# Kernel optimization log

Measured on AMD Instinct MI355X. Metric: run time of the kernel, lower is better.

## Reference

```python
import jax, jax.numpy as jnp
import numpy as np

B, L, N = 512, 512, 128


def setup_inputs() -> dict:
    key = jax.random.key(0)
    k1, k2, k3, k4 = jax.random.split(key, 4)
    emission = jax.random.normal(k1, (B, L, N), dtype=jnp.float32)
    target = jax.random.randint(k2, (B, L), 0, N, dtype=jnp.int32)
    mask = jnp.ones((B, L), dtype=jnp.float32)
    # params: uniform(-0.1, 0.1) as in reset_parameters
    start_trans = jax.random.uniform(k3, (N,), minval=-0.1, maxval=0.1, dtype=jnp.float32)
    trans = jax.random.uniform(k4, (N, N), minval=-0.1, maxval=0.1, dtype=jnp.float32)
    return {"emission": emission, "target": target, "mask": mask,
            "start_trans": start_trans, "trans": trans}


def _normalizer(emission, mask, start_trans, trans):
    # scores: [B, N]
    scores0 = start_trans + emission[:, 0]
    em_t = jnp.swapaxes(emission, 0, 1)[1:]          # [L-1, B, N]
    m_t = jnp.swapaxes(mask, 0, 1)[1:, :, None]      # [L-1, B, 1]

    def step(scores, xs):
        em_i, m_i = xs
        nxt = jax.nn.logsumexp(scores[:, :, None] + trans[None], axis=1) + em_i
        nxt = m_i * nxt + (1.0 - m_i) * scores
        return nxt, None

    final, _ = jax.lax.scan(step, scores0, (em_t, m_t))
    return jax.nn.logsumexp(final, axis=1)            # [B]


def _path_score(emission, target, mask, start_trans, trans):
    # mask*next + (1-mask)*scores == scores + mask*increment -> fully vectorizable
    b = jnp.arange(emission.shape[0])
    t0 = target[:, 0]
    s0 = start_trans[t0] + emission[b, 0, t0]                         # [B]
    prev, cur = target[:, :-1], target[:, 1:]                         # [B, L-1]
    em_gather = jnp.take_along_axis(emission[:, 1:], cur[:, :, None], axis=2)[..., 0]
    inc = trans[prev, cur] + em_gather                                # [B, L-1]
    return s0 + jnp.sum(mask[:, 1:] * inc, axis=1)                    # [B]


def reference(emission, target, mask, start_trans, trans):
    path_scores = _path_score(emission, target, mask, start_trans, trans)
    normalizer = _normalizer(emission, mask, start_trans, trans)
    return jnp.mean(normalizer - path_scores)
```

## Files before the change

kernel.cpp:

```cpp
#include <hip/hip_runtime.h>

#define B_ 512
#define L_ 512
#define N_ 128
#define TM 256
#define C_BIAS 3.0f

typedef _Float16 h2_t __attribute__((ext_vector_type(2)));

__device__ __forceinline__ float dot2f(h2_t a, h2_t b, float c) {
#if __has_builtin(__builtin_amdgcn_fdot2)
    return __builtin_amdgcn_fdot2(a, b, c, false);
#else
    return c + (float)a[0] * (float)b[0] + (float)a[1] * (float)b[1];
#endif
}

#define DPP_STEP_MAX(v, ctrl)                                                   \
    {                                                                           \
        int _t = __builtin_amdgcn_update_dpp(__float_as_int(v),                 \
                    __float_as_int(v), ctrl, 0xf, 0xf, false);                  \
        v = fmaxf(v, __int_as_float(_t));                                       \
    }
#define DPP_STEP_ADD(v, ctrl)                                                   \
    {                                                                           \
        int _t = __builtin_amdgcn_update_dpp(__float_as_int(v),                 \
                    __float_as_int(v), ctrl, 0xf, 0xf, false);                  \
        v = v + __int_as_float(_t);                                             \
    }

__device__ __forceinline__ float wave_max(float v) {
    DPP_STEP_MAX(v, 0xB1);
    DPP_STEP_MAX(v, 0x4E);
    DPP_STEP_MAX(v, 0x141);
    DPP_STEP_MAX(v, 0x140);
    DPP_STEP_MAX(v, 0x142);
    DPP_STEP_MAX(v, 0x143);
    return __int_as_float(__builtin_amdgcn_readlane(__float_as_int(v), 63));
}
__device__ __forceinline__ float wave_sum(float v) {
    DPP_STEP_ADD(v, 0xB1);
    DPP_STEP_ADD(v, 0x4E);
    DPP_STEP_ADD(v, 0x141);
    DPP_STEP_ADD(v, 0x140);
    DPP_STEP_ADD(v, 0x142);
    DPP_STEP_ADD(v, 0x143);
    return __int_as_float(__builtin_amdgcn_readlane(__float_as_int(v), 63));
}

__global__ __launch_bounds__(64) void norm_kernel(
    const float* __restrict__ em, const int* __restrict__ tg,
    const float* __restrict__ mask, const float* __restrict__ st,
    const float* __restrict__ trans,
    float* __restrict__ alpha, float* __restrict__ beta,
    float* __restrict__ pathf, float* __restrict__ pathb)
{
    __shared__ __align__(16) h2_t Eh[64];
    __shared__ float Mlds[TM];

    const int l  = threadIdx.x;
    const int b  = blockIdx.x >> 1;
    const int bw = blockIdx.x & 1;
    const size_t base = (size_t)b * L_ * N_;
    const int bL = b * L_;

    if (bw == 0) {
        float pacc = 0.f;
        for (int t = 1 + l; t < TM; t += 64) {
            int cur  = tg[bL + t];
            int prev = tg[bL + t - 1];
            pacc += mask[bL + t] * (trans[prev * N_ + cur] + em[base + (size_t)t * N_ + cur]);
        }
        pacc = wave_sum(pacc);
        if (l == 0) {
            int t0 = tg[bL];
            pathf[b] = pacc + st[t0] + em[base + t0];
        }

#pragma unroll
        for (int k = 0; k < 4; ++k) Mlds[l + 64 * k] = mask[bL + l + 64 * k];

        h2_t et0[64], et1[64];
#pragma unroll
        for (int k = 0; k < 64; ++k) {
            float2 r0 = *(const float2*)(trans + (2 * k    ) * N_ + 2 * l);
            float2 r1 = *(const float2*)(trans + (2 * k + 1) * N_ + 2 * l);
            h2_t a, c;
            a[0] = (_Float16)__expf(r0.x); a[1] = (_Float16)__expf(r1.x);
            c[0] = (_Float16)__expf(r0.y); c[1] = (_Float16)__expf(r1.y);
            et0[k] = a; et1[k] = c;
        }

        float2 e0 = *(const float2*)(em + base + 2 * l);
        float2 s2 = *(const float2*)(st + 2 * l);
        float ns0 = s2.x + e0.x;
        float ns1 = s2.y + e0.y;
        float Mprev = wave_max(fmaxf(ns0, ns1));
        {
            h2_t eo;
            eo[0] = (_Float16)__expf(ns0 - Mprev - C_BIAS);
            eo[1] = (_Float16)__expf(ns1 - Mprev - C_BIAS);
            Eh[l] = eo;
        }

        float2 pipe0 = *(const float2*)(em + base + (size_t)1 * N_ + 2 * l);
        float2 pipe1 = *(const float2*)(em + base + (size_t)2 * N_ + 2 * l);
        float2 pipe2 = *(const float2*)(em + base + (size_t)3 * N_ + 2 * l);
        float2 pipe3 = *(const float2*)(em + base + (size_t)4 * N_ + 2 * l);

        auto step = [&](int t, float2& slot) {
            float2 emv = slot;
            int tpf = t + 4; if (tpf > TM - 1) tpf = TM - 1;
            slot = *(const float2*)(em + base + (size_t)tpf * N_ + 2 * l);
            float mk = Mlds[t];

            float mx = wave_max(fmaxf(ns0, ns1));

            float a0 = 0.f, a1 = 0.f, a2 = 0.f, a3 = 0.f;
            float c0 = 0.f, c1 = 0.f, c2 = 0.f, c3 = 0.f;
            const float4* E4 = (const float4*)Eh;
#pragma unroll
            for (int r = 0; r < 16; ++r) {
                float4 blk = E4[r];
                const h2_t* e2 = (const h2_t*)&blk;
                a0 = dot2f(e2[0], et0[4 * r + 0], a0);
                a1 = dot2f(e2[1], et0[4 * r + 1], a1);
                a2 = dot2f(e2[2], et0[4 * r + 2], a2);
                a3 = dot2f(e2[3], et0[4 * r + 3], a3);
                c0 = dot2f(e2[0], et1[4 * r + 0], c0);
                c1 = dot2f(e2[1], et1[4 * r + 1], c1);
                c2 = dot2f(e2[2], et1[4 * r + 2], c2);
                c3 = dot2f(e2[3], et1[4 * r + 3], c3);
            }
            float s_0 = (a0 + a1) + (a2 + a3);
            float s_1 = (c0 + c1) + (c2 + c3);

            float badd = Mprev + C_BIAS;
            float nxt0 = __logf(s_0) + badd + emv.x;
            float nxt1 = __logf(s_1) + badd + emv.y;
            float im = 1.f - mk;
            ns0 = mk * nxt0 + im * ns0;
            ns1 = mk * nxt1 + im * ns1;

            Mprev = mx;
            h2_t eo;
            eo[0] = (_Float16)__expf(ns0 - mx - C_BIAS);
            eo[1] = (_Float16)__expf(ns1 - mx - C_BIAS);
            Eh[l] = eo;
        };

        for (int tt = 1; tt + 3 < TM; tt += 4) {
            step(tt    , pipe0);
            step(tt + 1, pipe1);
            step(tt + 2, pipe2);
            step(tt + 3, pipe3);
        }
        step(TM - 3, pipe0);
        step(TM - 2, pipe1);
        step(TM - 1, pipe2);

        *(float2*)(alpha + b * N_ + 2 * l) = make_float2(ns0, ns1);
    } else {
        float pacc = 0.f;
        for (int t = TM + l; t < L_; t += 64) {
            int cur  = tg[bL + t];
            int prev = tg[bL + t - 1];
            pacc += mask[bL + t] * (trans[prev * N_ + cur] + em[base + (size_t)t * N_ + cur]);
        }
        pacc = wave_sum(pacc);
        if (l == 0) pathb[b] = pacc;

#pragma unroll
        for (int k = 0; k < 4; ++k) Mlds[l + 64 * k] = mask[bL + TM + l + 64 * k];

        h2_t er0[64], er1[64];
#pragma unroll
        for (int k4 = 0; k4 < 32; ++k4) {
            float4 q0 = *(const float4*)(trans + (2 * l    ) * N_ + 4 * k4);
            float4 q1 = *(const float4*)(trans + (2 * l + 1) * N_ + 4 * k4);
            h2_t a, c;
            a[0] = (_Float16)__expf(q0.x); a[1] = (_Float16)__expf(q0.y);
            er0[2 * k4] = a;
            a[0] = (_Float16)__expf(q0.z); a[1] = (_Float16)__expf(q0.w);
            er0[2 * k4 + 1] = a;
            c[0] = (_Float16)__expf(q1.x); c[1] = (_Float16)__expf(q1.y);
            er1[2 * k4] = c;
            c[0] = (_Float16)__expf(q1.z); c[1] = (_Float16)__expf(q1.w);
            er1[2 * k4 + 1] = c;
        }

        float2 e0 = *(const float2*)(em + base + (size_t)(L_ - 1) * N_ + 2 * l);
        float b0 = 0.f, b1 = 0.f;
        float v0 = e0.x, v1 = e0.y;
        float Mprev = wave_max(fmaxf(v0, v1));
        {
            h2_t eo;
            eo[0] = (_Float16)__expf(v0 - Mprev - C_BIAS);
            eo[1] = (_Float16)__expf(v1 - Mprev - C_BIAS);
            Eh[l] = eo;
        }

        float2 pipe0 = *(const float2*)(em + base + (size_t)510 * N_ + 2 * l);
        float2 pipe1 = *(const float2*)(em + base + (size_t)509 * N_ + 2 * l);
        float2 pipe2 = *(const float2*)(em + base + (size_t)508 * N_ + 2 * l);
        float2 pipe3 = *(const float2*)(em + base + (size_t)507 * N_ + 2 * l);

        auto step = [&](int t, float2& slot) {
            float2 emt = slot;
            int tpf = t - 4; if (tpf < TM - 1) tpf = TM - 1;
            slot = *(const float2*)(em + base + (size_t)tpf * N_ + 2 * l);
            float mk = Mlds[t + 1 - TM];

            float mx = wave_max(fmaxf(v0, v1));

            float a0 = 0.f, a1 = 0.f, a2 = 0.f, a3 = 0.f;
            float c0 = 0.f, c1 = 0.f, c2 = 0.f, c3 = 0.f;
            const float4* F4 = (const float4*)Eh;
#pragma unroll
            for (int r = 0; r < 16; ++r) {
                float4 blk = F4[r];
                const h2_t* f2 = (const h2_t*)&blk;
                a0 = dot2f(f2[0], er0[4 * r + 0], a0);
                a1 = dot2f(f2[1], er0[4 * r + 1], a1);
                a2 = dot2f(f2[2], er0[4 * r + 2], a2);
                a3 = dot2f(f2[3], er0[4 * r + 3], a3);
                c0 = dot2f(f2[0], er1[4 * r + 0], c0);
                c1 = dot2f(f2[1], er1[4 * r + 1], c1);
                c2 = dot2f(f2[2], er1[4 * r + 2], c2);
                c3 = dot2f(f2[3], er1[4 * r + 3], c3);
            }
            float s_0 = (a0 + a1) + (a2 + a3);
            float s_1 = (c0 + c1) + (c2 + c3);

            float badd = Mprev + C_BIAS;
            float upd0 = __logf(s_0) + badd;
            float upd1 = __logf(s_1) + badd;
            float im = 1.f - mk;
            b0 = mk * upd0 + im * b0;
            b1 = mk * upd1 + im * b1;

            v0 = b0 + emt.x;
            v1 = b1 + emt.y;
            Mprev = mx;
            h2_t eo;
            eo[0] = (_Float16)__expf(v0 - mx - C_BIAS);
            eo[1] = (_Float16)__expf(v1 - mx - C_BIAS);
            Eh[l] = eo;
        };

        for (int tt = 510; tt >= 258; tt -= 4) {
            step(tt    , pipe0);
            step(tt - 1, pipe1);
            step(tt - 2, pipe2);
            step(tt - 3, pipe3);
        }

        *(float2*)(beta + b * N_ + 2 * l) = make_float2(b0, b1);
    }
}

__global__ __launch_bounds__(64) void zres_kernel(
    const float* __restrict__ alpha, const float* __restrict__ beta,
    const float* __restrict__ pathf, const float* __restrict__ pathb,
    float* __restrict__ zres)
{
    const int l = threadIdx.x;
    const int b = blockIdx.x;
    float2 av = *(const float2*)(alpha + b * N_ + 2 * l);
    float2 bv = *(const float2*)(beta  + b * N_ + 2 * l);
    float v0 = av.x + bv.x;
    float v1 = av.y + bv.y;
    float m = wave_max(fmaxf(v0, v1));
    float s = wave_sum(__expf(v0 - m) + __expf(v1 - m));
    if (l == 0) zres[b] = m + __logf(s) - pathf[b] - pathb[b];
}

__global__ __launch_bounds__(64) void mean_kernel(
    const float* __restrict__ zres, float* __restrict__ out)
{
    const int l = threadIdx.x;
    const float4* z4 = (const float4*)zres;
    float4 a = z4[2 * l];
    float4 c = z4[2 * l + 1];
    float acc = ((a.x + a.y) + (a.z + a.w)) + ((c.x + c.y) + (c.z + c.w));
    acc = wave_sum(acc);
    if (l == 0) out[0] = acc * (1.0f / (float)B_);
}

extern "C" void kernel_launch(void* const* d_in, const int* in_sizes, int n_in,
                              void* d_out, int out_size, void* d_ws, size_t ws_size,
                              hipStream_t stream) {
    const float* emission    = (const float*)d_in[0];
    const int*   target      = (const int*)  d_in[1];
    const float* mask        = (const float*)d_in[2];
    const float* start_trans = (const float*)d_in[3];
    const float* trans       = (const float*)d_in[4];
    float* out = (float*)d_out;

    float* ws_f  = (float*)d_ws;
    float* alpha = ws_f;
    float* beta  = ws_f + B_ * N_;
    float* pathf = ws_f + 2 * B_ * N_;
    float* pathb = ws_f + 2 * B_ * N_ + B_;
    float* zres  = ws_f + 2 * B_ * N_ + 2 * B_;

    norm_kernel<<<2 * B_, 64, 0, stream>>>(emission, target, mask, start_trans,
                                           trans, alpha, beta, pathf, pathb);
    zres_kernel<<<B_, 64, 0, stream>>>(alpha, beta, pathf, pathb, zres);
    mean_kernel<<<1, 64, 0, stream>>>(zres, out);
}
```

Baseline: 331.9 us.

## Split each CRF chain over two waves with double-buffered LDS and barriers

```diff
diff --git a/kernel.cpp b/kernel.cpp
--- a/kernel.cpp
+++ b/kernel.cpp
@@ -29,13 +29,17 @@
         v = v + __int_as_float(_t);                                             \
     }
 
-__device__ __forceinline__ float wave_max(float v) {
+__device__ __forceinline__ float wave_max63(float v) {
     DPP_STEP_MAX(v, 0xB1);
     DPP_STEP_MAX(v, 0x4E);
     DPP_STEP_MAX(v, 0x141);
     DPP_STEP_MAX(v, 0x140);
     DPP_STEP_MAX(v, 0x142);
     DPP_STEP_MAX(v, 0x143);
+    return v;
+}
+__device__ __forceinline__ float wave_max(float v) {
+    v = wave_max63(v);
     return __int_as_float(__builtin_amdgcn_readlane(__float_as_int(v), 63));
 }
 __device__ __forceinline__ float wave_sum(float v) {
@@ -48,105 +52,106 @@
     return __int_as_float(__builtin_amdgcn_readlane(__float_as_int(v), 63));
 }
 
-__global__ __launch_bounds__(64) void norm_kernel(
+__device__ __forceinline__ void sync_lds() {
+    asm volatile("s_waitcnt lgkmcnt(0)" ::: "memory");
+    __builtin_amdgcn_s_barrier();
+    asm volatile("" ::: "memory");
+}
+
+__global__ __launch_bounds__(128, 2) void norm_kernel(
     const float* __restrict__ em, const int* __restrict__ tg,
     const float* __restrict__ mask, const float* __restrict__ st,
     const float* __restrict__ trans,
     float* __restrict__ alpha, float* __restrict__ beta,
     float* __restrict__ pathf, float* __restrict__ pathb)
 {
-    __shared__ __align__(16) h2_t Eh[64];
+    __shared__ __align__(16) _Float16 Ebuf[2][128];
     __shared__ float Mlds[TM];
-
-    const int l  = threadIdx.x;
-    const int b  = blockIdx.x >> 1;
-    const int bw = blockIdx.x & 1;
+    __shared__ __align__(8) float Hm[2][2];
+    __shared__ float Psum[2];
+
+    const int tid = threadIdx.x;
+    const int w   = tid >> 6;
+    const int b   = blockIdx.x >> 1;
+    const int bw  = blockIdx.x & 1;
     const size_t base = (size_t)b * L_ * N_;
     const int bL = b * L_;
 
     if (bw == 0) {
         float pacc = 0.f;
-        for (int t = 1 + l; t < TM; t += 64) {
+        for (int t = 1 + tid; t < TM; t += 128) {
             int cur  = tg[bL + t];
             int prev = tg[bL + t - 1];
             pacc += mask[bL + t] * (trans[prev * N_ + cur] + em[base + (size_t)t * N_ + cur]);
         }
         pacc = wave_sum(pacc);
-        if (l == 0) {
+        if ((tid & 63) == 0) Psum[w] = pacc;
+
+#pragma unroll
+        for (int k = 0; k < 2; ++k) Mlds[tid + 128 * k] = mask[bL + tid + 128 * k];
+
+        h2_t et[64];
+#pragma unroll
+        for (int k = 0; k < 64; ++k) {
+            float r0 = trans[(2 * k    ) * N_ + tid];
+            float r1 = trans[(2 * k + 1) * N_ + tid];
+            h2_t a;
+            a[0] = (_Float16)__expf(r0); a[1] = (_Float16)__expf(r1);
+            et[k] = a;
+        }
+
+        float ns = st[tid] + em[base + tid];
+        {
+            float hl = wave_max63(ns);
+            if ((tid & 63) == 63) Hm[0][w] = hl;
+        }
+        sync_lds();
+        float gmax0 = fmaxf(Hm[0][0], Hm[0][1]);
+        float Mprev = gmax0;
+        Ebuf[0][tid] = (_Float16)__expf(ns - gmax0 - C_BIAS);
+        if (tid == 0) {
             int t0 = tg[bL];
-            pathf[b] = pacc + st[t0] + em[base + t0];
-        }
-
-#pragma unroll
-        for (int k = 0; k < 4; ++k) Mlds[l + 64 * k] = mask[bL + l + 64 * k];
-
-        h2_t et0[64], et1[64];
-#pragma unroll
-        for (int k = 0; k < 64; ++k) {
-            float2 r0 = *(const float2*)(trans + (2 * k    ) * N_ + 2 * l);
-            float2 r1 = *(const float2*)(trans + (2 * k + 1) * N_ + 2 * l);
-            h2_t a, c;
-            a[0] = (_Float16)__expf(r0.x); a[1] = (_Float16)__expf(r1.x);
-            c[0] = (_Float16)__expf(r0.y); c[1] = (_Float16)__expf(r1.y);
-            et0[k] = a; et1[k] = c;
-        }
-
-        float2 e0 = *(const float2*)(em + base + 2 * l);
-        float2 s2 = *(const float2*)(st + 2 * l);
-        float ns0 = s2.x + e0.x;
-        float ns1 = s2.y + e0.y;
-        float Mprev = wave_max(fmaxf(ns0, ns1));
-        {
-            h2_t eo;
-            eo[0] = (_Float16)__expf(ns0 - Mprev - C_BIAS);
-            eo[1] = (_Float16)__expf(ns1 - Mprev - C_BIAS);
-            Eh[l] = eo;
-        }
-
-        float2 pipe0 = *(const float2*)(em + base + (size_t)1 * N_ + 2 * l);
-        float2 pipe1 = *(const float2*)(em + base + (size_t)2 * N_ + 2 * l);
-        float2 pipe2 = *(const float2*)(em + base + (size_t)3 * N_ + 2 * l);
-        float2 pipe3 = *(const float2*)(em + base + (size_t)4 * N_ + 2 * l);
-
-        auto step = [&](int t, float2& slot) {
-            float2 emv = slot;
+            pathf[b] = Psum[0] + Psum[1] + st[t0] + em[base + t0];
+        }
+        sync_lds();
+
+        float pipe0 = em[base + (size_t)1 * N_ + tid];
+        float pipe1 = em[base + (size_t)2 * N_ + tid];
+        float pipe2 = em[base + (size_t)3 * N_ + tid];
+        float pipe3 = em[base + (size_t)4 * N_ + tid];
+
+        auto step = [&](int t, float& slot) {
+            float emv = slot;
             int tpf = t + 4; if (tpf > TM - 1) tpf = TM - 1;
-            slot = *(const float2*)(em + base + (size_t)tpf * N_ + 2 * l);
+            slot = em[base + (size_t)tpf * N_ + tid];
             float mk = Mlds[t];
-
-            float mx = wave_max(fmaxf(ns0, ns1));
+            const int cu = t & 1, pv = cu ^ 1;
+
+            float2 hm = *(const float2*)&Hm[pv][0];
+            float gmax = fmaxf(hm.x, hm.y);
 
             float a0 = 0.f, a1 = 0.f, a2 = 0.f, a3 = 0.f;
-            float c0 = 0.f, c1 = 0.f, c2 = 0.f, c3 = 0.f;
-            const float4* E4 = (const float4*)Eh;
+            const float4* E4 = (const float4*)(&Ebuf[pv][0]);
 #pragma unroll
             for (int r = 0; r < 16; ++r) {
                 float4 blk = E4[r];
                 const h2_t* e2 = (const h2_t*)&blk;
-                a0 = dot2f(e2[0], et0[4 * r + 0], a0);
-                a1 = dot2f(e2[1], et0[4 * r + 1], a1);
-                a2 = dot2f(e2[2], et0[4 * r + 2], a2);
-                a3 = dot2f(e2[3], et0[4 * r + 3], a3);
-                c0 = dot2f(e2[0], et1[4 * r + 0], c0);
-                c1 = dot2f(e2[1], et1[4 * r + 1], c1);
-                c2 = dot2f(e2[2], et1[4 * r + 2], c2);
-                c3 = dot2f(e2[3], et1[4 * r + 3], c3);
+                a0 = dot2f(e2[0], et[4 * r + 0], a0);
+                a1 = dot2f(e2[1], et[4 * r + 1], a1);
+                a2 = dot2f(e2[2], et[4 * r + 2], a2);
+                a3 = dot2f(e2[3], et[4 * r + 3], a3);
             }
-            float s_0 = (a0 + a1) + (a2 + a3);
-            float s_1 = (c0 + c1) + (c2 + c3);
-
-            float badd = Mprev + C_BIAS;
-            float nxt0 = __logf(s_0) + badd + emv.x;
-            float nxt1 = __logf(s_1) + badd + emv.y;
+            float s_ = (a0 + a1) + (a2 + a3);
+
+            float nxt = __logf(s_) + Mprev + C_BIAS + emv;
             float im = 1.f - mk;
-            ns0 = mk * nxt0 + im * ns0;
-            ns1 = mk * nxt1 + im * ns1;
-
-            Mprev = mx;
-            h2_t eo;
-            eo[0] = (_Float16)__expf(ns0 - mx - C_BIAS);
-            eo[1] = (_Float16)__expf(ns1 - mx - C_BIAS);
-            Eh[l] = eo;
+            ns = mk * nxt + im * ns;
+
+            float hl = wave_max63(ns);
+            if ((tid & 63) == 63) Hm[cu][w] = hl;
+            Ebuf[cu][tid] = (_Float16)__expf(ns - gmax - C_BIAS);
+            Mprev = gmax;
+            sync_lds();
         };
 
         for (int tt = 1; tt + 3 < TM; tt += 4) {
@@ -159,103 +164,92 @@
         step(TM - 2, pipe1);
         step(TM - 1, pipe2);
 
-        *(float2*)(alpha + b * N_ + 2 * l) = make_float2(ns0, ns1);
+        alpha[b * N_ + tid] = ns;
     } else {
         float pacc = 0.f;
-        for (int t = TM + l; t < L_; t += 64) {
+        for (int t = TM + tid; t < L_; t += 128) {
             int cur  = tg[bL + t];
             int prev = tg[bL + t - 1];
             pacc += mask[bL + t] * (trans[prev * N_ + cur] + em[base + (size_t)t * N_ + cur]);
         }
         pacc = wave_sum(pacc);
-        if (l == 0) pathb[b] = pacc;
-
-#pragma unroll
-        for (int k = 0; k < 4; ++k) Mlds[l + 64 * k] = mask[bL + TM + l + 64 * k];
-
-        h2_t er0[64], er1[64];
+        if ((tid & 63) == 0) Psum[w] = pacc;
+
+#pragma unroll
+        for (int k = 0; k < 2; ++k) Mlds[tid + 128 * k] = mask[bL + TM + tid + 128 * k];
+
+        h2_t er[64];
 #pragma unroll
         for (int k4 = 0; k4 < 32; ++k4) {
-            float4 q0 = *(const float4*)(trans + (2 * l    ) * N_ + 4 * k4);
-            float4 q1 = *(const float4*)(trans + (2 * l + 1) * N_ + 4 * k4);
-            h2_t a, c;
-            a[0] = (_Float16)__expf(q0.x); a[1] = (_Float16)__expf(q0.y);
-            er0[2 * k4] = a;
-            a[0] = (_Float16)__expf(q0.z); a[1] = (_Float16)__expf(q0.w);
-            er0[2 * k4 + 1] = a;
-            c[0] = (_Float16)__expf(q1.x); c[1] = (_Float16)__expf(q1.y);
-            er1[2 * k4] = c;
-            c[0] = (_Float16)__expf(q1.z); c[1] = (_Float16)__expf(q1.w);
-            er1[2 * k4 + 1] = c;
-        }
-
-        float2 e0 = *(const float2*)(em + base + (size_t)(L_ - 1) * N_ + 2 * l);
-        float b0 = 0.f, b1 = 0.f;
-        float v0 = e0.x, v1 = e0.y;
-        float Mprev = wave_max(fmaxf(v0, v1));
+            float4 q = *(const float4*)(trans + tid * N_ + 4 * k4);
+            h2_t a;
+            a[0] = (_Float16)__expf(q.x); a[1] = (_Float16)__expf(q.y);
+            er[2 * k4] = a;
+            a[0] = (_Float16)__expf(q.z); a[1] = (_Float16)__expf(q.w);
+            er[2 * k4 + 1] = a;
+        }
+
+        float bv = 0.f;
+        float v = em[base + (size_t)(L_ - 1) * N_ + tid];
         {
-            h2_t eo;
-            eo[0] = (_Float16)__expf(v0 - Mprev - C_BIAS);
-            eo[1] = (_Float16)__expf(v1 - Mprev - C_BIAS);
-            Eh[l] = eo;
-        }
-
-        float2 pipe0 = *(const float2*)(em + base + (size_t)510 * N_ + 2 * l);
-        float2 pipe1 = *(const float2*)(em + base + (size_t)509 * N_ + 2 * l);
-        float2 pipe2 = *(const float2*)(em + base + (size_t)508 * N_ + 2 * l);
-        float2 pipe3 = *(const float2*)(em + base + (size_t)507 * N_ + 2 * l);
-
-        auto step = [&](int t, float2& slot) {
-            float2 emt = slot;
-            int tpf = t - 4; if (tpf < TM - 1) tpf = TM - 1;
-            slot = *(const float2*)(em + base + (size_t)tpf * N_ + 2 * l);
-            float mk = Mlds[t + 1 - TM];
-
-            float mx = wave_max(fmaxf(v0, v1));
+            float hl = wave_max63(v);
+            if ((tid & 63) == 63) Hm[0][w] = hl;
+        }
+        sync_lds();
+        float gmax0 = fmaxf(Hm[0][0], Hm[0][1]);
+        float Mprev = gmax0;
+        Ebuf[0][tid] = (_Float16)__expf(v - gmax0 - C_BIAS);
+        if (tid == 0) pathb[b] = Psum[0] + Psum[1];
+        sync_lds();
+
+        float pipe0 = em[base + (size_t)510 * N_ + tid];
+        float pipe1 = em[base + (size_t)509 * N_ + tid];
+        float pipe2 = em[base + (size_t)508 * N_ + tid];
+        float pipe3 = em[base + (size_t)507 * N_ + tid];
+
+        auto step = [&](int u, float& slot) {
+            float emt = slot;
+            int tpf = u - 4; if (tpf < TM - 1) tpf = TM - 1;
+            slot = em[base + (size_t)tpf * N_ + tid];
+            float mk = Mlds[u + 1 - TM];
+            const int cu = (u & 1) ^ 1, pv = cu ^ 1;
+
+            float2 hm = *(const float2*)&Hm[pv][0];
+            float gmax = fmaxf(hm.x, hm.y);
 
             float a0 = 0.f, a1 = 0.f, a2 = 0.f, a3 = 0.f;
-            float c0 = 0.f, c1 = 0.f, c2 = 0.f, c3 = 0.f;
-            const float4* F4 = (const float4*)Eh;
+            const float4* F4 = (const float4*)(&Ebuf[pv][0]);
 #pragma unroll
             for (int r = 0; r < 16; ++r) {
                 float4 blk = F4[r];
                 const h2_t* f2 = (const h2_t*)&blk;
-                a0 = dot2f(f2[0], er0[4 * r + 0], a0);
-                a1 = dot2f(f2[1], er0[4 * r + 1], a1);
-                a2 = dot2f(f2[2], er0[4 * r + 2], a2);
-                a3 = dot2f(f2[3], er0[4 * r + 3], a3);
-                c0 = dot2f(f2[0], er1[4 * r + 0], c0);
-                c1 = dot2f(f2[1], er1[4 * r + 1], c1);
-                c2 = dot2f(f2[2], er1[4 * r + 2], c2);
-                c3 = dot2f(f2[3], er1[4 * r + 3], c3);
+                a0 = dot2f(f2[0], er[4 * r + 0], a0);
+                a1 = dot2f(f2[1], er[4 * r + 1], a1);
+                a2 = dot2f(f2[2], er[4 * r + 2], a2);
+                a3 = dot2f(f2[3], er[4 * r + 3], a3);
             }
-            float s_0 = (a0 + a1) + (a2 + a3);
-            float s_1 = (c0 + c1) + (c2 + c3);
-
-            float badd = Mprev + C_BIAS;
-            float upd0 = __logf(s_0) + badd;
-            float upd1 = __logf(s_1) + badd;
+            float s_ = (a0 + a1) + (a2 + a3);
+
+            float upd = __logf(s_) + Mprev + C_BIAS;
             float im = 1.f - mk;
-            b0 = mk * upd0 + im * b0;
-            b1 = mk * upd1 + im * b1;
-
-            v0 = b0 + emt.x;
-            v1 = b1 + emt.y;
-            Mprev = mx;
-            h2_t eo;
-            eo[0] = (_Float16)__expf(v0 - mx - C_BIAS);
-            eo[1] = (_Float16)__expf(v1 - mx - C_BIAS);
-            Eh[l] = eo;
+            bv = mk * upd + im * bv;
+
+            v = bv + emt;
+            float hl = wave_max63(v);
+            if ((tid & 63) == 63) Hm[cu][w] = hl;
+            Ebuf[cu][tid] = (_Float16)__expf(v - gmax - C_BIAS);
+            Mprev = gmax;
+            sync_lds();
         };
 
-        for (int tt = 510; tt >= 258; tt -= 4) {
-            step(tt    , pipe0);
-            step(tt - 1, pipe1);
-            step(tt - 2, pipe2);
-            step(tt - 3, pipe3);
-        }
-
-        *(float2*)(beta + b * N_ + 2 * l) = make_float2(b0, b1);
+        for (int uu = 510; uu >= 258; uu -= 4) {
+            step(uu    , pipe0);
+            step(uu - 1, pipe1);
+            step(uu - 2, pipe2);
+            step(uu - 3, pipe3);
+        }
+
+        beta[b * N_ + tid] = bv;
     }
 }
 
@@ -304,8 +298,8 @@
     float* pathb = ws_f + 2 * B_ * N_ + B_;
     float* zres  = ws_f + 2 * B_ * N_ + 2 * B_;
 
-    norm_kernel<<<2 * B_, 64, 0, stream>>>(emission, target, mask, start_trans,
-                                           trans, alpha, beta, pathf, pathb);
+    norm_kernel<<<2 * B_, 128, 0, stream>>>(emission, target, mask, start_trans,
+                                            trans, alpha, beta, pathf, pathb);
     zres_kernel<<<B_, 64, 0, stream>>>(alpha, beta, pathf, pathb, zres);
     mean_kernel<<<1, 64, 0, stream>>>(zres, out);
 }
```

Result: no change. 329.3 us (-0.8%).

## Replace fdot2 matvec in CRF forward/backward recursion with MFMA 16x16x32 f16

Applied to the files above, without the earlier changes.

```diff
diff --git a/kernel.cpp b/kernel.cpp
--- a/kernel.cpp
+++ b/kernel.cpp
@@ -7,14 +7,8 @@
 #define C_BIAS 3.0f
 
 typedef _Float16 h2_t __attribute__((ext_vector_type(2)));
-
-__device__ __forceinline__ float dot2f(h2_t a, h2_t b, float c) {
-#if __has_builtin(__builtin_amdgcn_fdot2)
-    return __builtin_amdgcn_fdot2(a, b, c, false);
-#else
-    return c + (float)a[0] * (float)b[0] + (float)a[1] * (float)b[1];
-#endif
-}
+typedef _Float16 h8_t __attribute__((ext_vector_type(8)));
+typedef float    f4_t __attribute__((ext_vector_type(4)));
 
 #define DPP_STEP_MAX(v, ctrl)                                                   \
     {                                                                           \
@@ -55,10 +49,13 @@
     float* __restrict__ alpha, float* __restrict__ beta,
     float* __restrict__ pathf, float* __restrict__ pathb)
 {
-    __shared__ __align__(16) h2_t Eh[64];
+    __shared__ __align__(16) _Float16 Eh[128];
+    __shared__ __align__(8)  float    Sl[128];
     __shared__ float Mlds[TM];
 
     const int l  = threadIdx.x;
+    const int c  = l & 15;
+    const int h  = l >> 4;
     const int b  = blockIdx.x >> 1;
     const int bw = blockIdx.x & 1;
     const size_t base = (size_t)b * L_ * N_;
@@ -80,16 +77,17 @@
 #pragma unroll
         for (int k = 0; k < 4; ++k) Mlds[l + 64 * k] = mask[bL + l + 64 * k];
 
-        h2_t et0[64], et1[64];
-#pragma unroll
-        for (int k = 0; k < 64; ++k) {
-            float2 r0 = *(const float2*)(trans + (2 * k    ) * N_ + 2 * l);
-            float2 r1 = *(const float2*)(trans + (2 * k + 1) * N_ + 2 * l);
-            h2_t a, c;
-            a[0] = (_Float16)__expf(r0.x); a[1] = (_Float16)__expf(r1.x);
-            c[0] = (_Float16)__expf(r0.y); c[1] = (_Float16)__expf(r1.y);
-            et0[k] = a; et1[k] = c;
-        }
+        h8_t Bf[8][4];
+#pragma unroll
+        for (int jt = 0; jt < 8; ++jt)
+#pragma unroll
+            for (int ks = 0; ks < 4; ++ks) {
+                h8_t f;
+#pragma unroll
+                for (int e = 0; e < 8; ++e)
+                    f[e] = (_Float16)__expf(trans[(32 * ks + 8 * h + e) * N_ + 16 * jt + c]);
+                Bf[jt][ks] = f;
+            }
 
         float2 e0 = *(const float2*)(em + base + 2 * l);
         float2 s2 = *(const float2*)(st + 2 * l);
@@ -100,7 +98,7 @@
             h2_t eo;
             eo[0] = (_Float16)__expf(ns0 - Mprev - C_BIAS);
             eo[1] = (_Float16)__expf(ns1 - Mprev - C_BIAS);
-            Eh[l] = eo;
+            ((h2_t*)Eh)[l] = eo;
         }
 
         float2 pipe0 = *(const float2*)(em + base + (size_t)1 * N_ + 2 * l);
@@ -116,28 +114,31 @@
 
             float mx = wave_max(fmaxf(ns0, ns1));
 
-            float a0 = 0.f, a1 = 0.f, a2 = 0.f, a3 = 0.f;
-            float c0 = 0.f, c1 = 0.f, c2 = 0.f, c3 = 0.f;
-            const float4* E4 = (const float4*)Eh;
-#pragma unroll
-            for (int r = 0; r < 16; ++r) {
-                float4 blk = E4[r];
-                const h2_t* e2 = (const h2_t*)&blk;
-                a0 = dot2f(e2[0], et0[4 * r + 0], a0);
-                a1 = dot2f(e2[1], et0[4 * r + 1], a1);
-                a2 = dot2f(e2[2], et0[4 * r + 2], a2);
-                a3 = dot2f(e2[3], et0[4 * r + 3], a3);
-                c0 = dot2f(e2[0], et1[4 * r + 0], c0);
-                c1 = dot2f(e2[1], et1[4 * r + 1], c1);
-                c2 = dot2f(e2[2], et1[4 * r + 2], c2);
-                c3 = dot2f(e2[3], et1[4 * r + 3], c3);
-            }
-            float s_0 = (a0 + a1) + (a2 + a3);
-            float s_1 = (c0 + c1) + (c2 + c3);
+            const _Float16* Eb = (const _Float16*)Eh;
+            h8_t A0 = *(const h8_t*)(Eb + 8 * h);
+            h8_t A1 = *(const h8_t*)(Eb + 32 + 8 * h);
+            h8_t A2 = *(const h8_t*)(Eb + 64 + 8 * h);
+            h8_t A3 = *(const h8_t*)(Eb + 96 + 8 * h);
+
+            f4_t z = {0.f, 0.f, 0.f, 0.f};
+            f4_t acc[8];
+#pragma unroll
+            for (int jt = 0; jt < 8; ++jt) {
+                f4_t a = __builtin_amdgcn_mfma_f32_16x16x32_f16(A0, Bf[jt][0], z, 0, 0, 0);
+                a = __builtin_amdgcn_mfma_f32_16x16x32_f16(A1, Bf[jt][1], a, 0, 0, 0);
+                a = __builtin_amdgcn_mfma_f32_16x16x32_f16(A2, Bf[jt][2], a, 0, 0, 0);
+                a = __builtin_amdgcn_mfma_f32_16x16x32_f16(A3, Bf[jt][3], a, 0, 0, 0);
+                acc[jt] = a;
+            }
+            if (l < 16) {
+#pragma unroll
+                for (int jt = 0; jt < 8; ++jt) Sl[16 * jt + c] = acc[jt][0];
+            }
+            float2 sv = *(const float2*)(Sl + 2 * l);
 
             float badd = Mprev + C_BIAS;
-            float nxt0 = __logf(s_0) + badd + emv.x;
-            float nxt1 = __logf(s_1) + badd + emv.y;
+            float nxt0 = __logf(sv.x) + badd + emv.x;
+            float nxt1 = __logf(sv.y) + badd + emv.y;
             float im = 1.f - mk;
             ns0 = mk * nxt0 + im * ns0;
             ns1 = mk * nxt1 + im * ns1;
@@ -146,7 +147,7 @@
             h2_t eo;
             eo[0] = (_Float16)__expf(ns0 - mx - C_BIAS);
             eo[1] = (_Float16)__expf(ns1 - mx - C_BIAS);
-            Eh[l] = eo;
+            ((h2_t*)Eh)[l] = eo;
         };
 
         for (int tt = 1; tt + 3 < TM; tt += 4) {
@@ -173,21 +174,21 @@
 #pragma unroll
         for (int k = 0; k < 4; ++k) Mlds[l + 64 * k] = mask[bL + TM + l + 64 * k];
 
-        h2_t er0[64], er1[64];
-#pragma unroll
-        for (int k4 = 0; k4 < 32; ++k4) {
-            float4 q0 = *(const float4*)(trans + (2 * l    ) * N_ + 4 * k4);
-            float4 q1 = *(const float4*)(trans + (2 * l + 1) * N_ + 4 * k4);
-            h2_t a, c;
-            a[0] = (_Float16)__expf(q0.x); a[1] = (_Float16)__expf(q0.y);
-            er0[2 * k4] = a;
-            a[0] = (_Float16)__expf(q0.z); a[1] = (_Float16)__expf(q0.w);
-            er0[2 * k4 + 1] = a;
-            c[0] = (_Float16)__expf(q1.x); c[1] = (_Float16)__expf(q1.y);
-            er1[2 * k4] = c;
-            c[0] = (_Float16)__expf(q1.z); c[1] = (_Float16)__expf(q1.w);
-            er1[2 * k4 + 1] = c;
-        }
+        h8_t Bf[8][4];
+#pragma unroll
+        for (int it = 0; it < 8; ++it)
+#pragma unroll
+            for (int ks = 0; ks < 4; ++ks) {
+                const float* p = trans + (size_t)(16 * it + c) * N_ + 32 * ks + 8 * h;
+                float4 q0 = *(const float4*)p;
+                float4 q1 = *(const float4*)(p + 4);
+                h8_t f;
+                f[0] = (_Float16)__expf(q0.x); f[1] = (_Float16)__expf(q0.y);
+                f[2] = (_Float16)__expf(q0.z); f[3] = (_Float16)__expf(q0.w);
+                f[4] = (_Float16)__expf(q1.x); f[5] = (_Float16)__expf(q1.y);
+                f[6] = (_Float16)__expf(q1.z); f[7] = (_Float16)__expf(q1.w);
+                Bf[it][ks] = f;
+            }
 
         float2 e0 = *(const float2*)(em + base + (size_t)(L_ - 1) * N_ + 2 * l);
         float b0 = 0.f, b1 = 0.f;
@@ -197,7 +198,7 @@
             h2_t eo;
             eo[0] = (_Float16)__expf(v0 - Mprev - C_BIAS);
             eo[1] = (_Float16)__expf(v1 - Mprev - C_BIAS);
-            Eh[l] = eo;
+            ((h2_t*)Eh)[l] = eo;
         }
 
         float2 pipe0 = *(const float2*)(em + base + (size_t)510 * N_ + 2 * l);
@@ -213,28 +214,31 @@
 
             float mx = wave_max(fmaxf(v0, v1));
 
-            float a0 = 0.f, a1 = 0.f, a2 = 0.f, a3 = 0.f;
-            float c0 = 0.f, c1 = 0.f, c2 = 0.f, c3 = 0.f;
-            const float4* F4 = (const float4*)Eh;
-#pragma unroll
-            for (int r = 0; r < 16; ++r) {
-                float4 blk = F4[r];
-                const h2_t* f2 = (const h2_t*)&blk;
-                a0 = dot2f(f2[0], er0[4 * r + 0], a0);
-                a1 = dot2f(f2[1], er0[4 * r + 1], a1);
-                a2 = dot2f(f2[2], er0[4 * r + 2], a2);
-                a3 = dot2f(f2[3], er0[4 * r + 3], a3);
-                c0 = dot2f(f2[0], er1[4 * r + 0], c0);
-                c1 = dot2f(f2[1], er1[4 * r + 1], c1);
-                c2 = dot2f(f2[2], er1[4 * r + 2], c2);
-                c3 = dot2f(f2[3], er1[4 * r + 3], c3);
-            }
-            float s_0 = (a0 + a1) + (a2 + a3);
-            float s_1 = (c0 + c1) + (c2 + c3);
+            const _Float16* Fb = (const _Float16*)Eh;
+            h8_t A0 = *(const h8_t*)(Fb + 8 * h);
+            h8_t A1 = *(const h8_t*)(Fb + 32 + 8 * h);
+            h8_t A2 = *(const h8_t*)(Fb + 64 + 8 * h);
+            h8_t A3 = *(const h8_t*)(Fb + 96 + 8 * h);
+
+            f4_t z = {0.f, 0.f, 0.f, 0.f};
+            f4_t acc[8];
+#pragma unroll
+            for (int it = 0; it < 8; ++it) {
+                f4_t a = __builtin_amdgcn_mfma_f32_16x16x32_f16(A0, Bf[it][0], z, 0, 0, 0);
+                a = __builtin_amdgcn_mfma_f32_16x16x32_f16(A1, Bf[it][1], a, 0, 0, 0);
+                a = __builtin_amdgcn_mfma_f32_16x16x32_f16(A2, Bf[it][2], a, 0, 0, 0);
+                a = __builtin_amdgcn_mfma_f32_16x16x32_f16(A3, Bf[it][3], a, 0, 0, 0);
+                acc[it] = a;
+            }
+            if (l < 16) {
+#pragma unroll
+                for (int it = 0; it < 8; ++it) Sl[16 * it + c] = acc[it][0];
+            }
+            float2 sv = *(const float2*)(Sl + 2 * l);
 
             float badd = Mprev + C_BIAS;
-            float upd0 = __logf(s_0) + badd;
-            float upd1 = __logf(s_1) + badd;
+            float upd0 = __logf(sv.x) + badd;
+            float upd1 = __logf(sv.y) + badd;
             float im = 1.f - mk;
             b0 = mk * upd0 + im * b0;
             b1 = mk * upd1 + im * b1;
@@ -245,7 +249,7 @@
             h2_t eo;
             eo[0] = (_Float16)__expf(v0 - mx - C_BIAS);
             eo[1] = (_Float16)__expf(v1 - mx - C_BIAS);
-            Eh[l] = eo;
+            ((h2_t*)Eh)[l] = eo;
         };
 
         for (int tt = 510; tt >= 258; tt -= 4) {
```

Measured after the change: 302.7 us. 8.8% less time.
